# Performance work log

Measured on AMD Instinct MI355X. Metric: run time of the kernel, lower is better.

Reference implementation:

```python
import jax, jax.numpy as jnp
import numpy as np

N = 16384            # mesh vertices at full resolution (level 3)
DEG = 8              # avg nonzeros per Laplacian row
F_IN = 3
F_HID = 128
LOCAL_LAYERS = 15
LEVEL_N = [N >> (3 - l) for l in range(4)]  # [2048, 4096, 8192, 16384]


def setup_inputs():
    key = jax.random.key(0)
    ks = iter(jax.random.split(key, 48))
    d = {}
    d['inputs'] = jax.random.normal(next(ks), (1, N, F_IN), dtype=jnp.float32)
    d['mask0'] = jnp.ones((1, N, 1), jnp.float32)
    d['mask1'] = jnp.ones((1, N, 1), jnp.float32)
    for l, n in enumerate(LEVEL_N):
        e = DEG * n
        d[f'lap{l}_rows'] = jnp.sort(jax.random.randint(next(ks), (e,), 0, n, dtype=jnp.int32))
        d[f'lap{l}_cols'] = jax.random.randint(next(ks), (e,), 0, n, dtype=jnp.int32)
        d[f'lap{l}_vals'] = 0.25 * jax.random.normal(next(ks), (e,), dtype=jnp.float32)
    e = DEG * N
    d['L_rows'] = jnp.sort(jax.random.randint(next(ks), (e,), 0, N, dtype=jnp.int32))
    d['L_cols'] = jax.random.randint(next(ks), (e,), 0, N, dtype=jnp.int32)
    d['L_vals'] = 0.25 * jax.random.normal(next(ks), (e,), dtype=jnp.float32)
    s_in = 0.577   # ~1/sqrt(F_IN)
    s_h = 0.0625   # 1/sqrt(2*F_HID)
    d['g_conv1_W'] = s_in * jax.random.normal(next(ks), (F_IN, F_HID), dtype=jnp.float32)
    d['g_conv1_b'] = jnp.zeros((F_HID,), jnp.float32)
    d['g_down_W'] = s_h * jax.random.normal(next(ks), (3, 2, 2 * F_HID, F_HID), dtype=jnp.float32)
    d['g_down_b'] = jnp.zeros((3, 2, F_HID), jnp.float32)
    d['g_lap0_W'] = s_h * jax.random.normal(next(ks), (2, 2 * F_HID, F_HID), dtype=jnp.float32)
    d['g_lap0_b'] = jnp.zeros((2, F_HID), jnp.float32)
    d['g_up_W'] = s_h * jax.random.normal(next(ks), (3, 2, 2 * F_HID, F_HID), dtype=jnp.float32)
    d['g_up_b'] = jnp.zeros((3, 2, F_HID), jnp.float32)
    d['g_conv2_W'] = s_h * jax.random.normal(next(ks), (F_HID, 2), dtype=jnp.float32)
    d['g_conv2_b'] = jnp.zeros((2,), jnp.float32)
    d['l_conv1_W'] = s_in * jax.random.normal(next(ks), (F_IN, F_HID), dtype=jnp.float32)
    d['l_conv1_b'] = jnp.zeros((F_HID,), jnp.float32)
    d['l_rn_W'] = s_h * jax.random.normal(next(ks), (LOCAL_LAYERS, 2, 2 * F_HID, F_HID), dtype=jnp.float32)
    d['l_rn_b'] = jnp.zeros((LOCAL_LAYERS, 2, F_HID), jnp.float32)
    d['l_conv2_W'] = s_h * jax.random.normal(next(ks), (F_HID, 1), dtype=jnp.float32)
    d['l_conv2_b'] = jnp.zeros((1,), jnp.float32)
    return d


def _spmm(rows, cols, vals, x):
    # y = L @ x for an n x n COO Laplacian; x: [1, n, f] (batch=1, sparse mm path)
    y = jax.ops.segment_sum(vals[:, None] * x[0, cols, :], rows, num_segments=x.shape[1])
    return y[None]


def _lap_block(lap, x, Ws, bs):
    # _LapResNet2 (num_outputs == num_inputs == 128): elu -> cat([x, Lx]) -> 1x1 conv, residual
    inp = x
    for j in range(Ws.shape[0]):
        x = jax.nn.elu(x)
        x = jnp.concatenate([x, _spmm(lap[0], lap[1], lap[2], x)], axis=-1) @ Ws[j] + bs[j]
    return x + inp


def _avg_block(mask, x, Ws, bs):
    # _AvgResNet2: elu -> cat([x, masked global average]) -> 1x1 conv, residual
    inp = x
    denom = jnp.sum(mask, axis=1, keepdims=True)
    for j in range(Ws.shape[0]):
        x = jax.nn.elu(x)
        avg = jnp.sum(x * mask, axis=1, keepdims=True) / denom
        x = jnp.concatenate([x, jnp.broadcast_to(avg, x.shape)], axis=-1) @ Ws[j] + bs[j]
    return x + inp


def _maxpool2(x):
    # MaxPool1d(2, stride=2) along the node dim
    b, n, f = x.shape
    return x.reshape(b, n // 2, 2, f).max(axis=2)


def _forward(inputs, mask0, mask1, lap0_vals, lap1_vals, lap2_vals, lap3_vals, L_vals,
             g_conv1_W, g_conv1_b, g_down_W, g_down_b, g_lap0_W, g_lap0_b,
             g_up_W, g_up_b, g_conv2_W, g_conv2_b,
             l_conv1_W, l_conv1_b, l_rn_W, l_rn_b, l_conv2_W, l_conv2_b,
             lap0_rows, lap0_cols, lap1_rows, lap1_cols, lap2_rows, lap2_cols,
             lap3_rows, lap3_cols, L_rows, L_cols):
    laps = [(lap0_rows, lap0_cols, lap0_vals), (lap1_rows, lap1_cols, lap1_vals),
            (lap2_rows, lap2_cols, lap2_vals), (lap3_rows, lap3_cols, lap3_vals)]
    # ----- global net: EfficientCascade (naive max-pool cascade, 4 levels) -----
    # (mask0 is only max-pooled in torch; _LapResNet2 ignores it, so it does not affect math)
    x = inputs @ g_conv1_W + g_conv1_b
    down = []
    for k, i in enumerate((3, 2, 1)):
        down.append(x)
        x = _lap_block(laps[i], x, g_down_W[k], g_down_b[k])
        x = _maxpool2(x)
    x = _lap_block(laps[0], x, g_lap0_W, g_lap0_b)
    for i in (1, 2, 3):
        x = jnp.repeat(x, 2, axis=1)      # F.interpolate(scale_factor=2), nearest
        x = x + down[-i]                  # channels equal -> plain residual add
        x = _lap_block(laps[i], x, g_up_W[i - 1], g_up_b[i - 1])
    swg = jax.nn.elu(x) @ g_conv2_W + g_conv2_b + inputs[:, :, :2]  # + repeating_expand(inputs, 2)
    # ----- local net: LapDeepModel, 15 alternating Lap / global-avg resblocks -----
    L = (L_rows, L_cols, L_vals)
    y = inputs @ l_conv1_W + l_conv1_b
    for i in range(LOCAL_LAYERS):
        if i % 2 == 0:
            y = _lap_block(L, y, l_rn_W[i], l_rn_b[i])
        else:
            y = _avg_block(mask1, y, l_rn_W[i], l_rn_b[i])
    score_local = jax.nn.elu(y) @ l_conv2_W + l_conv2_b + inputs[:, :, :1]
    # ----- combine -----
    score_global = swg[:, :, :1]
    weight_global = jax.nn.sigmoid(swg[:, :, :-1])  # out_features=1 -> same first channel
    score_final = weight_global * score_global + (1.0 - weight_global) * score_local
    return jnp.concatenate([score_global, score_local, score_final], axis=1)


def reference(inputs, mask0, mask1, lap0_rows, lap0_cols, lap0_vals,
              lap1_rows, lap1_cols, lap1_vals, lap2_rows, lap2_cols, lap2_vals,
              lap3_rows, lap3_cols, lap3_vals, L_rows, L_cols, L_vals,
              g_conv1_W, g_conv1_b, g_down_W, g_down_b, g_lap0_W, g_lap0_b,
              g_up_W, g_up_b, g_conv2_W, g_conv2_b,
              l_conv1_W, l_conv1_b, l_rn_W, l_rn_b, l_conv2_W, l_conv2_b):
    return _forward(inputs, mask0, mask1, lap0_vals, lap1_vals, lap2_vals, lap3_vals, L_vals,
                    g_conv1_W, g_conv1_b, g_down_W, g_down_b, g_lap0_W, g_lap0_b,
                    g_up_W, g_up_b, g_conv2_W, g_conv2_b,
                    l_conv1_W, l_conv1_b, l_rn_W, l_rn_b, l_conv2_W, l_conv2_b,
                    lap0_rows, lap0_cols, lap1_rows, lap1_cols, lap2_rows, lap2_cols,
                    lap3_rows, lap3_cols, L_rows, L_cols)
```

## Files before the change

kernel.cpp:

```cpp
#include <hip/hip_runtime.h>

#define F 128
#define SPAD 136
#define NR 32

typedef __attribute__((ext_vector_type(8))) short short8;
typedef __attribute__((ext_vector_type(16))) float f32x16;
typedef unsigned long long ull;

__device__ __forceinline__ float elu_f(float x) {
    return x > 0.f ? x : __expf(x) - 1.f;
}
__device__ __forceinline__ ushort f2bf(float x) {
    unsigned u = __float_as_uint(x);
    u = (u + 0x7FFFu + ((u >> 16) & 1u)) >> 16;
    return (ushort)u;
}
__device__ __forceinline__ float bf2f(ushort u) {
    return __uint_as_float((unsigned)u << 16);
}
__device__ __forceinline__ void bfma8(float* a, float v, short8 u) {
#pragma unroll
    for (int i = 0; i < 8; ++i) a[i] += v * bf2f((ushort)u[i]);
}

struct SetupArgs {
    const float* ws0; const float* ws1; const float* ws2; const float* ws3;
    ushort* wd0; ushort* wd1; ushort* wd2; ushort* wd3;
    const int* rows0; const int* rows1; const int* rows2; const int* rows3; const int* rows4;
    int* rp0; int* rp1; int* rp2; int* rp3; int* rp4;
    const float* mask; float* den; float* acc;
};

__global__ __launch_bounds__(256) void setup_kernel(SetupArgs s) {
    __shared__ ushort tile[16384];
    int b = blockIdx.x, t = threadIdx.x;
    if (b < 88) {
        const float* src; ushort* dst; int lb;
        if (b < 12)      { src = s.ws0; dst = s.wd0; lb = b; }
        else if (b < 16) { src = s.ws1; dst = s.wd1; lb = b - 12; }
        else if (b < 28) { src = s.ws2; dst = s.wd2; lb = b - 16; }
        else             { src = s.ws3; dst = s.wd3; lb = b - 28; }
        src += (size_t)lb * 16384; dst += (size_t)lb * 16384;
        for (int idx = t; idx < 16384; idx += 256) {
            int k = idx >> 7, nn = idx & 127;
            int k0 = k >> 4, rk = k & 15, j = rk & 7, lh = rk >> 3;
            int n0 = nn >> 5, ll = nn & 31;
            tile[((k0 * 4 + n0) * 64 + lh * 32 + ll) * 8 + j] = f2bf(src[idx]);
        }
        __syncthreads();
        ull* td = (ull*)dst; const ull* ts = (const ull*)tile;
        for (int i = t; i < 4096; i += 256) td[i] = ts[i];
    } else if (b < 273) {
        int tid = (b - 88) * 256 + t;
        const int ns[5] = {2048, 4096, 8192, 16384, 16384};
        const int es[5] = {16384, 32768, 65536, 131072, 131072};
        const int* rowsA[5] = {s.rows0, s.rows1, s.rows2, s.rows3, s.rows4};
        int* rpA[5] = {s.rp0, s.rp1, s.rp2, s.rp3, s.rp4};
        int base = 0;
        for (int lv = 0; lv < 5; ++lv) {
            int cnt = ns[lv] + 1;
            if (tid < base + cnt) {
                int r = tid - base;
                const int* rows = rowsA[lv]; int e = es[lv];
                int lo = 0, hi = e;
                while (lo < hi) { int mid = (lo + hi) >> 1; if (rows[mid] < r) lo = mid + 1; else hi = mid; }
                rpA[lv][r] = lo;
                return;
            }
            base += cnt;
        }
    } else {
        __shared__ float red[256];
        float ssum = 0.f;
        for (int i = t; i < 16384; i += 256) ssum += s.mask[i];
        red[t] = ssum; __syncthreads();
        for (int st = 128; st > 0; st >>= 1) { if (t < st) red[t] += red[t + st]; __syncthreads(); }
        if (t == 0) s.den[0] = red[0];
        for (int i = t; i < 14336; i += 256) s.acc[i] = 0.f;
    }
}

__global__ void conv1_dual(const float* __restrict__ in,
                           const float* __restrict__ Wg, const float* __restrict__ bg,
                           const float* __restrict__ Wl, const float* __restrict__ bl,
                           float* __restrict__ og, ushort* __restrict__ eg,
                           float* __restrict__ ol, ushort* __restrict__ el, int n) {
    int id = blockIdx.x * 256 + threadIdx.x;
    if (id >= n * F) return;
    int r = id >> 7, c = id & 127;
    float x0 = in[r * 3 + 0], x1 = in[r * 3 + 1], x2 = in[r * 3 + 2];
    float g = x0 * Wg[c] + x1 * Wg[F + c] + x2 * Wg[2 * F + c] + bg[c];
    float lo = x0 * Wl[c] + x1 * Wl[F + c] + x2 * Wl[2 * F + c] + bl[c];
    og[id] = g;  eg[id] = f2bf(elu_f(g));
    ol[id] = lo; el[id] = f2bf(elu_f(lo));
}

struct LArgs {
    const ushort* EA; const float* RES; float* OUT; ushort* EAOUT;
    const int* rowptr; const int* cols; const float* vals;
    const ushort* Wp; const float* bias;
    const float* accin; const float* den;
    const float* mask; float* accout;
    float* EO; ushort* EE; const float* SKIP;
    int epi;
    int fin;
    const float* Finp; const ushort* FEB0;
    const float* FgW2; const float* Fgb2; const float* FlW2; const float* Flb2;
    float* Fout;
};

__device__ __forceinline__ void layer_body(const LArgs& a, int blk, ushort* SS, float* FS) {
    const int t = threadIdx.x;
    const int rbase = blk * NR;
    const int w = t >> 6, l = t & 63, m = l & 31, kh = l >> 5;
    const int col = w * 32 + m;
    const bool lap = (a.rowptr != nullptr);
    const bool avg = (a.accin != nullptr);

    short8 afrag[8];
    {
        const ushort* ear = a.EA + (size_t)(rbase + m) * F + kh * 8;
#pragma unroll
        for (int ki = 0; ki < 8; ++ki) afrag[ki] = *(const short8*)(ear + ki * 16);
    }

    if (lap) {
        const int grp = t >> 3, l8 = t & 7;
        const short8* EA8 = (const short8*)a.EA;
        const int chunk = l8 * 2;
        int row = rbase + grp;
        int e0 = a.rowptr[row], e1 = a.rowptr[row + 1];
        float acc0[16], acc1[16];
#pragma unroll
        for (int i = 0; i < 16; ++i) { acc0[i] = 0.f; acc1[i] = 0.f; }
        int e = e0;
        for (; e + 4 <= e1; e += 4) {
            int c0 = a.cols[e + 0], c1 = a.cols[e + 1], c2 = a.cols[e + 2], c3 = a.cols[e + 3];
            float v0 = a.vals[e + 0], v1 = a.vals[e + 1], v2 = a.vals[e + 2], v3 = a.vals[e + 3];
            short8 u0a = EA8[(size_t)c0 * 16 + chunk], u0b = EA8[(size_t)c0 * 16 + chunk + 1];
            short8 u1a = EA8[(size_t)c1 * 16 + chunk], u1b = EA8[(size_t)c1 * 16 + chunk + 1];
            short8 u2a = EA8[(size_t)c2 * 16 + chunk], u2b = EA8[(size_t)c2 * 16 + chunk + 1];
            short8 u3a = EA8[(size_t)c3 * 16 + chunk], u3b = EA8[(size_t)c3 * 16 + chunk + 1];
            bfma8(acc0, v0, u0a); bfma8(acc0 + 8, v0, u0b);
            bfma8(acc1, v1, u1a); bfma8(acc1 + 8, v1, u1b);
            bfma8(acc0, v2, u2a); bfma8(acc0 + 8, v2, u2b);
            bfma8(acc1, v3, u3a); bfma8(acc1 + 8, v3, u3b);
        }
        for (; e < e1; ++e) {
            int cc = a.cols[e];
            float v = a.vals[e];
            short8 ua = EA8[(size_t)cc * 16 + chunk], ub = EA8[(size_t)cc * 16 + chunk + 1];
            bfma8(acc0, v, ua); bfma8(acc0 + 8, v, ub);
        }
        short8 s0, s1;
#pragma unroll
        for (int i = 0; i < 8; ++i) {
            s0[i] = (short)f2bf(acc0[i] + acc1[i]);
            s1[i] = (short)f2bf(acc0[8 + i] + acc1[8 + i]);
        }
        *(short8*)(&SS[grp * SPAD + l8 * 16]) = s0;
        *(short8*)(&SS[grp * SPAD + l8 * 16 + 8]) = s1;
        __syncthreads();
    } else if (avg) {
        if (t < 128) {
            float s = 0.f;
#pragma unroll
            for (int r = 0; r < 8; ++r) s += a.accin[r * 128 + t];
            SS[t] = f2bf(s / a.den[0]);
        }
        __syncthreads();
    }

    f32x16 acc;
#pragma unroll
    for (int i = 0; i < 16; ++i) acc[i] = 0.f;
#pragma unroll
    for (int ki = 0; ki < 8; ++ki) {
        short8 b = *(const short8*)(a.Wp + (size_t)(((ki * 4 + w) * 64 + l) * 8));
        acc = __builtin_amdgcn_mfma_f32_32x32x16_bf16(afrag[ki], b, acc, 0, 0, 0);
    }
    if (lap || avg) {
        const ushort* esr = lap ? &SS[m * SPAD + kh * 8] : &SS[kh * 8];
#pragma unroll
        for (int ki = 0; ki < 8; ++ki) {
            short8 aa = *(const short8*)(esr + ki * 16);
            short8 b = *(const short8*)(a.Wp + 16384 + (size_t)(((ki * 4 + w) * 64 + l) * 8));
            acc = __builtin_amdgcn_mfma_f32_32x32x16_bf16(aa, b, acc, 0, 0, 0);
        }
    }

    const float bv = a.bias[col];
    float outv[16];
#pragma unroll
    for (int reg = 0; reg < 16; ++reg) {
        int r = (reg & 3) + 8 * (reg >> 2) + 4 * kh;
        size_t rg = (size_t)(rbase + r);
        float v = acc[reg] + bv;
        if (a.RES) v += a.RES[rg * F + col];
        outv[reg] = v;
        if (a.OUT) a.OUT[rg * F + col] = v;
        if (a.EAOUT) a.EAOUT[rg * F + col] = f2bf(elu_f(v));
    }
    if (a.accout) {
        float p = 0.f;
#pragma unroll
        for (int reg = 0; reg < 16; ++reg) {
            int r = (reg & 3) + 8 * (reg >> 2) + 4 * kh;
            p += elu_f(outv[reg]) * a.mask[rbase + r];
        }
        p += __shfl_xor(p, 32, 64);
        if (l < 32) atomicAdd(a.accout + (blk & 7) * 128 + col, p);
    }
    if (a.epi == 1) {
        int rb2 = rbase >> 1;
#pragma unroll
        for (int q = 0; q < 4; ++q)
#pragma unroll
            for (int e2 = 0; e2 < 2; ++e2) {
                float pv = fmaxf(outv[q * 4 + e2 * 2], outv[q * 4 + e2 * 2 + 1]);
                size_t idx = (size_t)(rb2 + q * 4 + kh * 2 + e2) * F + col;
                a.EO[idx] = pv;
                a.EE[idx] = f2bf(elu_f(pv));
            }
    } else if (a.epi == 2) {
#pragma unroll
        for (int reg = 0; reg < 16; ++reg) {
            int r = (reg & 3) + 8 * (reg >> 2) + 4 * kh;
            size_t R0 = (size_t)(2 * (rbase + r)) * F + col;
            float v0 = outv[reg] + a.SKIP[R0];
            float v1 = outv[reg] + a.SKIP[R0 + F];
            a.EO[R0] = v0;     a.EO[R0 + F] = v1;
            a.EE[R0] = f2bf(elu_f(v0)); a.EE[R0 + F] = f2bf(elu_f(v1));
        }
    }
    if (a.fin) {
        __syncthreads();
        if (t < 64) FS[t] = 0.f;
        __syncthreads();
        const float lw = a.FlW2[col];
#pragma unroll
        for (int reg = 0; reg < 16; ++reg) {
            int r = (reg & 3) + 8 * (reg >> 2) + 4 * kh;
            atomicAdd(&FS[r], elu_f(outv[reg]) * lw);
        }
        for (int idx = t; idx < 32 * 128; idx += 256) {
            int r = idx >> 7, cc = idx & 127;
            atomicAdd(&FS[32 + r], bf2f(a.FEB0[(size_t)(rbase + r) * F + cc]) * a.FgW2[2 * cc]);
        }
        __syncthreads();
        if (t < 32) {
            int rg = rbase + t;
            float base = a.Finp[rg * 3 + 0];
            float sg = FS[32 + t] + a.Fgb2[0] + base;
            float sl = FS[t] + a.Flb2[0] + base;
            float wg = 1.f / (1.f + __expf(-sg));
            a.Fout[rg] = sg;
            a.Fout[16384 + rg] = sl;
            a.Fout[32768 + rg] = wg * sg + (1.f - wg) * sl;
        }
    }
}

__global__ __launch_bounds__(256)
void dual_layer(LArgs A, LArgs B, int nA) {
    __shared__ ushort SS[NR * SPAD];
    __shared__ float FS[64];
    bool isA = (int)blockIdx.x < nA;
    const LArgs& a = isA ? A : B;
    int blk = isA ? blockIdx.x : blockIdx.x - nA;
    layer_body(a, blk, SS, FS);
}

extern "C" void kernel_launch(void* const* d_in, const int* in_sizes, int n_in,
                              void* d_out, int out_size, void* d_ws, size_t ws_size,
                              hipStream_t stream) {
    (void)in_sizes; (void)n_in; (void)out_size; (void)ws_size;
    const float* inputs = (const float*)d_in[0];
    const float* mask1  = (const float*)d_in[2];
    const int*   lrows[5] = {(const int*)d_in[3], (const int*)d_in[6], (const int*)d_in[9],
                             (const int*)d_in[12], (const int*)d_in[15]};
    const int*   lcols[5] = {(const int*)d_in[4], (const int*)d_in[7], (const int*)d_in[10],
                             (const int*)d_in[13], (const int*)d_in[16]};
    const float* lvals[5] = {(const float*)d_in[5], (const float*)d_in[8], (const float*)d_in[11],
                             (const float*)d_in[14], (const float*)d_in[17]};
    const float* gW1 = (const float*)d_in[18];
    const float* gb1 = (const float*)d_in[19];
    const float* gdW = (const float*)d_in[20];
    const float* gdb = (const float*)d_in[21];
    const float* glW = (const float*)d_in[22];
    const float* glb = (const float*)d_in[23];
    const float* guW = (const float*)d_in[24];
    const float* gub = (const float*)d_in[25];
    const float* gW2 = (const float*)d_in[26];
    const float* gb2 = (const float*)d_in[27];
    const float* lW1 = (const float*)d_in[28];
    const float* lb1 = (const float*)d_in[29];
    const float* lrW = (const float*)d_in[30];
    const float* lrb = (const float*)d_in[31];
    const float* lW2 = (const float*)d_in[32];
    const float* lb2 = (const float*)d_in[33];
    float* out = (float*)d_out;

    const int N = 16384;
    const int nlev[5] = {2048, 4096, 8192, 16384, 16384};

    char* ws = (char*)d_ws;
    size_t off = 0;
    auto alloc = [&](size_t bytes) -> char* {
        char* p = ws + off;
        off = (off + bytes + 255) & ~(size_t)255;
        return p;
    };
    float* BUF0 = (float*)alloc((size_t)N * F * 4);
    float* GU   = (float*)alloc((size_t)N * F * 4);
    float* G2   = (float*)alloc((size_t)N * F * 4);
    float* D8   = (float*)alloc((size_t)8192 * F * 4);
    float* D4   = (float*)alloc((size_t)4096 * F * 4);
    float* D2   = (float*)alloc((size_t)2048 * F * 4);
    float* LB   = (float*)alloc((size_t)N * F * 4);
    ushort* EB0 = (ushort*)alloc((size_t)N * F * 2);
    ushort* EG1 = (ushort*)alloc((size_t)N * F * 2);
    ushort* EG2 = (ushort*)alloc((size_t)N * F * 2);
    ushort* ED8 = (ushort*)alloc((size_t)8192 * F * 2);
    ushort* ED4 = (ushort*)alloc((size_t)4096 * F * 2);
    ushort* ED2 = (ushort*)alloc((size_t)2048 * F * 2);
    ushort* LE1 = (ushort*)alloc((size_t)N * F * 2);
    ushort* LE2 = (ushort*)alloc((size_t)N * F * 2);
    int* rp[5];
    for (int i = 0; i < 5; ++i) rp[i] = (int*)alloc((size_t)(nlev[i] + 1) * 4);
    float* ACC = (float*)alloc((size_t)14 * 8 * 128 * 4);
    float* DEN = (float*)alloc(4);
    ushort* Pd = (ushort*)alloc((size_t)12 * 16384 * 2);
    ushort* Pl = (ushort*)alloc((size_t)4  * 16384 * 2);
    ushort* Pu = (ushort*)alloc((size_t)12 * 16384 * 2);
    ushort* Pr = (ushort*)alloc((size_t)60 * 16384 * 2);

    SetupArgs sa;
    sa.ws0 = gdW; sa.ws1 = glW; sa.ws2 = guW; sa.ws3 = lrW;
    sa.wd0 = Pd;  sa.wd1 = Pl;  sa.wd2 = Pu;  sa.wd3 = Pr;
    sa.rows0 = lrows[0]; sa.rows1 = lrows[1]; sa.rows2 = lrows[2];
    sa.rows3 = lrows[3]; sa.rows4 = lrows[4];
    sa.rp0 = rp[0]; sa.rp1 = rp[1]; sa.rp2 = rp[2]; sa.rp3 = rp[3]; sa.rp4 = rp[4];
    sa.mask = mask1; sa.den = DEN; sa.acc = ACC;
    setup_kernel<<<274, 256, 0, stream>>>(sa);

    conv1_dual<<<8192, 256, 0, stream>>>(inputs, gW1, gb1, lW1, lb1, BUF0, EB0, LB, LE1, N);

    const size_t PSZ = 2 * 16384;

    auto mkL = [&](const ushort* ea, const float* res, float* o, ushort* eao,
                   int lv, const ushort* wp, const float* bias, float* accout,
                   int epi, float* eo, ushort* ee, const float* skip,
                   const float* accin, int fin) {
        LArgs x;
        x.EA = ea; x.RES = res; x.OUT = o; x.EAOUT = eao;
        x.rowptr = (lv >= 0) ? rp[lv] : nullptr;
        x.cols = (lv >= 0) ? lcols[lv] : nullptr;
        x.vals = (lv >= 0) ? lvals[lv] : nullptr;
        x.Wp = wp; x.bias = bias;
        x.accin = accin; x.den = DEN;
        x.mask = mask1; x.accout = accout;
        x.EO = eo; x.EE = ee; x.SKIP = skip; x.epi = epi;
        x.fin = fin;
        x.Finp = inputs; x.FEB0 = EB0;
        x.FgW2 = gW2; x.Fgb2 = gb2; x.FlW2 = lW2; x.Flb2 = lb2; x.Fout = out;
        return x;
    };

    LArgs gs[14]; int gn[14];
    gs[0]  = mkL(EB0, 0, 0, EG1, 3, Pd + 0 * PSZ, gdb + 0,   0, 0, 0, 0, 0, 0, 0);  gn[0]  = 16384;
    gs[1]  = mkL(EG1, BUF0, 0, 0, 3, Pd + 1 * PSZ, gdb + 128, 0, 1, D8, ED8, 0, 0, 0); gn[1] = 16384;
    gs[2]  = mkL(ED8, 0, 0, EG1, 2, Pd + 2 * PSZ, gdb + 256, 0, 0, 0, 0, 0, 0, 0);  gn[2]  = 8192;
    gs[3]  = mkL(EG1, D8, 0, 0, 2, Pd + 3 * PSZ, gdb + 384, 0, 1, D4, ED4, 0, 0, 0); gn[3]  = 8192;
    gs[4]  = mkL(ED4, 0, 0, EG1, 1, Pd + 4 * PSZ, gdb + 512, 0, 0, 0, 0, 0, 0, 0);  gn[4]  = 4096;
    gs[5]  = mkL(EG1, D4, 0, 0, 1, Pd + 5 * PSZ, gdb + 640, 0, 1, D2, ED2, 0, 0, 0); gn[5]  = 4096;
    gs[6]  = mkL(ED2, 0, 0, EG1, 0, Pl + 0 * PSZ, glb + 0,   0, 0, 0, 0, 0, 0, 0);  gn[6]  = 2048;
    gs[7]  = mkL(EG1, D2, 0, 0, 0, Pl + 1 * PSZ, glb + 128, 0, 2, GU, EG2, D4, 0, 0); gn[7] = 2048;
    gs[8]  = mkL(EG2, 0, 0, EG1, 1, Pu + 0 * PSZ, gub + 0,   0, 0, 0, 0, 0, 0, 0);  gn[8]  = 4096;
    gs[9]  = mkL(EG1, GU, 0, 0, 1, Pu + 1 * PSZ, gub + 128, 0, 2, G2, EG2, D8, 0, 0); gn[9] = 4096;
    gs[10] = mkL(EG2, 0, 0, EG1, 2, Pu + 2 * PSZ, gub + 256, 0, 0, 0, 0, 0, 0, 0);  gn[10] = 8192;
    gs[11] = mkL(EG1, G2, 0, 0, 2, Pu + 3 * PSZ, gub + 384, 0, 2, GU, EG2, BUF0, 0, 0); gn[11] = 8192;
    gs[12] = mkL(EG2, 0, 0, EG1, 3, Pu + 4 * PSZ, gub + 512, 0, 0, 0, 0, 0, 0, 0);  gn[12] = 16384;
    gs[13] = mkL(EG1, GU, 0, EB0, 3, Pu + 5 * PSZ, gub + 640, 0, 0, 0, 0, 0, 0, 0); gn[13] = 16384;

    int gi = 0;
    auto launchLap = [&](const LArgs& loc) {
        if (gi < 14) {
            int na = gn[gi] / NR;
            dual_layer<<<na + 512, 256, 0, stream>>>(gs[gi], loc, na);
            ++gi;
        } else {
            dual_layer<<<512, 256, 0, stream>>>(loc, loc, 512);
        }
    };

    for (int i = 0; i < 15; ++i) {
        const ushort* P1 = Pr + (size_t)(2 * i) * PSZ;
        const ushort* P2 = Pr + (size_t)(2 * i + 1) * PSZ;
        const float* b1 = lrb + (size_t)i * 256;
        const float* b2 = b1 + 128;
        if ((i & 1) == 0) {
            LArgs s1 = mkL(LE1, 0, 0, LE2, 4, P1, b1, 0, 0, 0, 0, 0, 0, 0);
            float* accout = (i <= 12) ? (ACC + (size_t)i * 1024) : nullptr;
            int fin = (i == 14);
            LArgs s2 = mkL(LE2, LB, fin ? nullptr : LB, fin ? nullptr : LE1, 4,
                           P2, b2, accout, 0, 0, 0, 0, 0, fin);
            launchLap(s1);
            launchLap(s2);
        } else {
            LArgs s1 = mkL(LE1, 0, 0, LE2, -1, P1, b1, ACC + (size_t)i * 1024,
                           0, 0, 0, 0, ACC + (size_t)(i - 1) * 1024, 0);
            LArgs s2 = mkL(LE2, LB, LB, LE1, -1, P2, b2, 0,
                           0, 0, 0, 0, ACC + (size_t)i * 1024, 0);
            launchLap(s1);
            launchLap(s2);
        }
    }
}
```

Baseline: 684.7 us.

## Bucket rows by degree for balanced SpMM blocks and use nontemporal memory ops

Adds a counting-sort pass, fused into the conv1 kernel, that builds per-level row permutations ordered by nonzero count. Laplacian layer blocks then process 32 rows of similar degree, so the threads in a block do not wait on one long row. It also switches column/value loads, residual/skip loads and the output stores to nontemporal variants to reduce cache pollution. The costs are an extra shared-memory sync per block, scattered row writes in the epilogue instead of contiguous ones, and nontemporal streaming of data the next layer may want to reuse from L2.

```diff
diff --git a/kernel.cpp b/kernel.cpp
--- a/kernel.cpp
+++ b/kernel.cpp
@@ -23,6 +23,10 @@
 #pragma unroll
     for (int i = 0; i < 8; ++i) a[i] += v * bf2f((ushort)u[i]);
 }
+__device__ __forceinline__ float ldnt(const float* p) { return __builtin_nontemporal_load(p); }
+__device__ __forceinline__ int   ldnti(const int* p)  { return __builtin_nontemporal_load(p); }
+__device__ __forceinline__ void stnt(float* p, float v)   { __builtin_nontemporal_store(v, p); }
+__device__ __forceinline__ void stnt(ushort* p, ushort v) { __builtin_nontemporal_store(v, p); }
 
 struct SetupArgs {
     const float* ws0; const float* ws1; const float* ws2; const float* ws3;
@@ -81,19 +85,47 @@
     }
 }
 
-__global__ void conv1_dual(const float* __restrict__ in,
-                           const float* __restrict__ Wg, const float* __restrict__ bg,
-                           const float* __restrict__ Wl, const float* __restrict__ bl,
-                           float* __restrict__ og, ushort* __restrict__ eg,
-                           float* __restrict__ ol, ushort* __restrict__ el, int n) {
-    int id = blockIdx.x * 256 + threadIdx.x;
-    if (id >= n * F) return;
-    int r = id >> 7, c = id & 127;
-    float x0 = in[r * 3 + 0], x1 = in[r * 3 + 1], x2 = in[r * 3 + 2];
-    float g = x0 * Wg[c] + x1 * Wg[F + c] + x2 * Wg[2 * F + c] + bg[c];
-    float lo = x0 * Wl[c] + x1 * Wl[F + c] + x2 * Wl[2 * F + c] + bl[c];
-    og[id] = g;  eg[id] = f2bf(elu_f(g));
-    ol[id] = lo; el[id] = f2bf(elu_f(lo));
+struct CArgs {
+    const float* in; const float* Wg; const float* bg; const float* Wl; const float* bl;
+    float* og; ushort* eg; float* ol; ushort* el;
+    const int* rp0; const int* rp1; const int* rp2; const int* rp3; const int* rp4;
+    int* pm0; int* pm1; int* pm2; int* pm3; int* pm4;
+};
+
+__global__ __launch_bounds__(256) void conv1_perm(CArgs c) {
+    int b = blockIdx.x, t = threadIdx.x;
+    if (b < 8192) {
+        int id = b * 256 + t;
+        int r = id >> 7, cc = id & 127;
+        float x0 = c.in[r * 3 + 0], x1 = c.in[r * 3 + 1], x2 = c.in[r * 3 + 2];
+        float g = x0 * c.Wg[cc] + x1 * c.Wg[F + cc] + x2 * c.Wg[2 * F + cc] + c.bg[cc];
+        float lo = x0 * c.Wl[cc] + x1 * c.Wl[F + cc] + x2 * c.Wl[2 * F + cc] + c.bl[cc];
+        c.og[id] = g;  c.eg[id] = f2bf(elu_f(g));
+        c.ol[id] = lo; c.el[id] = f2bf(elu_f(lo));
+    } else {
+        int lv = b - 8192;
+        const int ns[5] = {2048, 4096, 8192, 16384, 16384};
+        const int* rpA[5] = {c.rp0, c.rp1, c.rp2, c.rp3, c.rp4};
+        int* pmA[5] = {c.pm0, c.pm1, c.pm2, c.pm3, c.pm4};
+        int n = ns[lv];
+        const int* rp = rpA[lv];
+        int* pm = pmA[lv];
+        __shared__ int hist[64];
+        if (t < 64) hist[t] = 0;
+        __syncthreads();
+        for (int r = t; r < n; r += 256) {
+            int d = rp[r + 1] - rp[r]; if (d > 63) d = 63;
+            atomicAdd(&hist[d], 1);
+        }
+        __syncthreads();
+        if (t == 0) { int s = 0; for (int i = 0; i < 64; ++i) { int h = hist[i]; hist[i] = s; s += h; } }
+        __syncthreads();
+        for (int r = t; r < n; r += 256) {
+            int d = rp[r + 1] - rp[r]; if (d > 63) d = 63;
+            int pos = atomicAdd(&hist[d], 1);
+            pm[pos] = r;
+        }
+    }
 }
 
 struct LArgs {
@@ -103,6 +135,7 @@
     const float* accin; const float* den;
     const float* mask; float* accout;
     float* EO; ushort* EE; const float* SKIP;
+    const int* perm;
     int epi;
     int fin;
     const float* Finp; const ushort* FEB0;
@@ -110,7 +143,8 @@
     float* Fout;
 };
 
-__device__ __forceinline__ void layer_body(const LArgs& a, int blk, ushort* SS, float* FS) {
+__device__ __forceinline__ void layer_body(const LArgs& a, int blk, ushort* SS,
+                                           float* FS, int* PR) {
     const int t = threadIdx.x;
     const int rbase = blk * NR;
     const int w = t >> 6, l = t & 63, m = l & 31, kh = l >> 5;
@@ -118,9 +152,12 @@
     const bool lap = (a.rowptr != nullptr);
     const bool avg = (a.accin != nullptr);
 
+    if (t < 32) PR[t] = a.perm ? a.perm[rbase + t] : rbase + t;
+    __syncthreads();
+
     short8 afrag[8];
     {
-        const ushort* ear = a.EA + (size_t)(rbase + m) * F + kh * 8;
+        const ushort* ear = a.EA + (size_t)PR[m] * F + kh * 8;
 #pragma unroll
         for (int ki = 0; ki < 8; ++ki) afrag[ki] = *(const short8*)(ear + ki * 16);
     }
@@ -129,15 +166,17 @@
         const int grp = t >> 3, l8 = t & 7;
         const short8* EA8 = (const short8*)a.EA;
         const int chunk = l8 * 2;
-        int row = rbase + grp;
+        int row = PR[grp];
         int e0 = a.rowptr[row], e1 = a.rowptr[row + 1];
         float acc0[16], acc1[16];
 #pragma unroll
         for (int i = 0; i < 16; ++i) { acc0[i] = 0.f; acc1[i] = 0.f; }
         int e = e0;
         for (; e + 4 <= e1; e += 4) {
-            int c0 = a.cols[e + 0], c1 = a.cols[e + 1], c2 = a.cols[e + 2], c3 = a.cols[e + 3];
-            float v0 = a.vals[e + 0], v1 = a.vals[e + 1], v2 = a.vals[e + 2], v3 = a.vals[e + 3];
+            int c0 = ldnti(a.cols + e + 0), c1 = ldnti(a.cols + e + 1);
+            int c2 = ldnti(a.cols + e + 2), c3 = ldnti(a.cols + e + 3);
+            float v0 = ldnt(a.vals + e + 0), v1 = ldnt(a.vals + e + 1);
+            float v2 = ldnt(a.vals + e + 2), v3 = ldnt(a.vals + e + 3);
             short8 u0a = EA8[(size_t)c0 * 16 + chunk], u0b = EA8[(size_t)c0 * 16 + chunk + 1];
             short8 u1a = EA8[(size_t)c1 * 16 + chunk], u1b = EA8[(size_t)c1 * 16 + chunk + 1];
             short8 u2a = EA8[(size_t)c2 * 16 + chunk], u2b = EA8[(size_t)c2 * 16 + chunk + 1];
@@ -148,8 +187,8 @@
             bfma8(acc1, v3, u3a); bfma8(acc1 + 8, v3, u3b);
         }
         for (; e < e1; ++e) {
-            int cc = a.cols[e];
-            float v = a.vals[e];
+            int cc = ldnti(a.cols + e);
+            float v = ldnt(a.vals + e);
             short8 ua = EA8[(size_t)cc * 16 + chunk], ub = EA8[(size_t)cc * 16 + chunk + 1];
             bfma8(acc0, v, ua); bfma8(acc0 + 8, v, ub);
         }
@@ -195,19 +234,19 @@
 #pragma unroll
     for (int reg = 0; reg < 16; ++reg) {
         int r = (reg & 3) + 8 * (reg >> 2) + 4 * kh;
-        size_t rg = (size_t)(rbase + r);
+        size_t rg = (size_t)PR[r];
         float v = acc[reg] + bv;
-        if (a.RES) v += a.RES[rg * F + col];
+        if (a.RES) v += ldnt(a.RES + rg * F + col);
         outv[reg] = v;
-        if (a.OUT) a.OUT[rg * F + col] = v;
-        if (a.EAOUT) a.EAOUT[rg * F + col] = f2bf(elu_f(v));
+        if (a.OUT) stnt(a.OUT + rg * F + col, v);
+        if (a.EAOUT) stnt(a.EAOUT + rg * F + col, f2bf(elu_f(v)));
     }
     if (a.accout) {
         float p = 0.f;
 #pragma unroll
         for (int reg = 0; reg < 16; ++reg) {
             int r = (reg & 3) + 8 * (reg >> 2) + 4 * kh;
-            p += elu_f(outv[reg]) * a.mask[rbase + r];
+            p += elu_f(outv[reg]) * a.mask[PR[r]];
         }
         p += __shfl_xor(p, 32, 64);
         if (l < 32) atomicAdd(a.accout + (blk & 7) * 128 + col, p);
@@ -220,18 +259,18 @@
             for (int e2 = 0; e2 < 2; ++e2) {
                 float pv = fmaxf(outv[q * 4 + e2 * 2], outv[q * 4 + e2 * 2 + 1]);
                 size_t idx = (size_t)(rb2 + q * 4 + kh * 2 + e2) * F + col;
-                a.EO[idx] = pv;
-                a.EE[idx] = f2bf(elu_f(pv));
+                stnt(a.EO + idx, pv);
+                stnt(a.EE + idx, f2bf(elu_f(pv)));
             }
     } else if (a.epi == 2) {
 #pragma unroll
         for (int reg = 0; reg < 16; ++reg) {
             int r = (reg & 3) + 8 * (reg >> 2) + 4 * kh;
             size_t R0 = (size_t)(2 * (rbase + r)) * F + col;
-            float v0 = outv[reg] + a.SKIP[R0];
-            float v1 = outv[reg] + a.SKIP[R0 + F];
-            a.EO[R0] = v0;     a.EO[R0 + F] = v1;
-            a.EE[R0] = f2bf(elu_f(v0)); a.EE[R0 + F] = f2bf(elu_f(v1));
+            float v0 = outv[reg] + ldnt(a.SKIP + R0);
+            float v1 = outv[reg] + ldnt(a.SKIP + R0 + F);
+            stnt(a.EO + R0, v0);     stnt(a.EO + R0 + F, v1);
+            stnt(a.EE + R0, f2bf(elu_f(v0))); stnt(a.EE + R0 + F, f2bf(elu_f(v1)));
         }
     }
     if (a.fin) {
@@ -246,11 +285,11 @@
         }
         for (int idx = t; idx < 32 * 128; idx += 256) {
             int r = idx >> 7, cc = idx & 127;
-            atomicAdd(&FS[32 + r], bf2f(a.FEB0[(size_t)(rbase + r) * F + cc]) * a.FgW2[2 * cc]);
+            atomicAdd(&FS[32 + r], bf2f(a.FEB0[(size_t)PR[r] * F + cc]) * a.FgW2[2 * cc]);
         }
         __syncthreads();
         if (t < 32) {
-            int rg = rbase + t;
+            int rg = PR[t];
             float base = a.Finp[rg * 3 + 0];
             float sg = FS[32 + t] + a.Fgb2[0] + base;
             float sl = FS[t] + a.Flb2[0] + base;
@@ -266,10 +305,11 @@
 void dual_layer(LArgs A, LArgs B, int nA) {
     __shared__ ushort SS[NR * SPAD];
     __shared__ float FS[64];
+    __shared__ int PR[32];
     bool isA = (int)blockIdx.x < nA;
     const LArgs& a = isA ? A : B;
     int blk = isA ? blockIdx.x : blockIdx.x - nA;
-    layer_body(a, blk, SS, FS);
+    layer_body(a, blk, SS, FS, PR);
 }
 
 extern "C" void kernel_launch(void* const* d_in, const int* in_sizes, int n_in,
@@ -329,6 +369,8 @@
     ushort* LE2 = (ushort*)alloc((size_t)N * F * 2);
     int* rp[5];
     for (int i = 0; i < 5; ++i) rp[i] = (int*)alloc((size_t)(nlev[i] + 1) * 4);
+    int* pm[5];
+    for (int i = 0; i < 5; ++i) pm[i] = (int*)alloc((size_t)nlev[i] * 4);
     float* ACC = (float*)alloc((size_t)14 * 8 * 128 * 4);
     float* DEN = (float*)alloc(4);
     ushort* Pd = (ushort*)alloc((size_t)12 * 16384 * 2);
@@ -345,14 +387,19 @@
     sa.mask = mask1; sa.den = DEN; sa.acc = ACC;
     setup_kernel<<<274, 256, 0, stream>>>(sa);
 
-    conv1_dual<<<8192, 256, 0, stream>>>(inputs, gW1, gb1, lW1, lb1, BUF0, EB0, LB, LE1, N);
+    CArgs ca;
+    ca.in = inputs; ca.Wg = gW1; ca.bg = gb1; ca.Wl = lW1; ca.bl = lb1;
+    ca.og = BUF0; ca.eg = EB0; ca.ol = LB; ca.el = LE1;
+    ca.rp0 = rp[0]; ca.rp1 = rp[1]; ca.rp2 = rp[2]; ca.rp3 = rp[3]; ca.rp4 = rp[4];
+    ca.pm0 = pm[0]; ca.pm1 = pm[1]; ca.pm2 = pm[2]; ca.pm3 = pm[3]; ca.pm4 = pm[4];
+    conv1_perm<<<8197, 256, 0, stream>>>(ca);
 
     const size_t PSZ = 2 * 16384;
 
     auto mkL = [&](const ushort* ea, const float* res, float* o, ushort* eao,
                    int lv, const ushort* wp, const float* bias, float* accout,
                    int epi, float* eo, ushort* ee, const float* skip,
-                   const float* accin, int fin) {
+                   const float* accin, int fin, const int* perm) {
         LArgs x;
         x.EA = ea; x.RES = res; x.OUT = o; x.EAOUT = eao;
         x.rowptr = (lv >= 0) ? rp[lv] : nullptr;
@@ -361,7 +408,7 @@
         x.Wp = wp; x.bias = bias;
         x.accin = accin; x.den = DEN;
         x.mask = mask1; x.accout = accout;
-        x.EO = eo; x.EE = ee; x.SKIP = skip; x.epi = epi;
+        x.EO = eo; x.EE = ee; x.SKIP = skip; x.perm = perm; x.epi = epi;
         x.fin = fin;
         x.Finp = inputs; x.FEB0 = EB0;
         x.FgW2 = gW2; x.Fgb2 = gb2; x.FlW2 = lW2; x.Flb2 = lb2; x.Fout = out;
@@ -369,20 +416,20 @@
     };
 
     LArgs gs[14]; int gn[14];
-    gs[0]  = mkL(EB0, 0, 0, EG1, 3, Pd + 0 * PSZ, gdb + 0,   0, 0, 0, 0, 0, 0, 0);  gn[0]  = 16384;
-    gs[1]  = mkL(EG1, BUF0, 0, 0, 3, Pd + 1 * PSZ, gdb + 128, 0, 1, D8, ED8, 0, 0, 0); gn[1] = 16384;
-    gs[2]  = mkL(ED8, 0, 0, EG1, 2, Pd + 2 * PSZ, gdb + 256, 0, 0, 0, 0, 0, 0, 0);  gn[2]  = 8192;
-    gs[3]  = mkL(EG1, D8, 0, 0, 2, Pd + 3 * PSZ, gdb + 384, 0, 1, D4, ED4, 0, 0, 0); gn[3]  = 8192;
-    gs[4]  = mkL(ED4, 0, 0, EG1, 1, Pd + 4 * PSZ, gdb + 512, 0, 0, 0, 0, 0, 0, 0);  gn[4]  = 4096;
-    gs[5]  = mkL(EG1, D4, 0, 0, 1, Pd + 5 * PSZ, gdb + 640, 0, 1, D2, ED2, 0, 0, 0); gn[5]  = 4096;
-    gs[6]  = mkL(ED2, 0, 0, EG1, 0, Pl + 0 * PSZ, glb + 0,   0, 0, 0, 0, 0, 0, 0);  gn[6]  = 2048;
-    gs[7]  = mkL(EG1, D2, 0, 0, 0, Pl + 1 * PSZ, glb + 128, 0, 2, GU, EG2, D4, 0, 0); gn[7] = 2048;
-    gs[8]  = mkL(EG2, 0, 0, EG1, 1, Pu + 0 * PSZ, gub + 0,   0, 0, 0, 0, 0, 0, 0);  gn[8]  = 4096;
-    gs[9]  = mkL(EG1, GU, 0, 0, 1, Pu + 1 * PSZ, gub + 128, 0, 2, G2, EG2, D8, 0, 0); gn[9] = 4096;
-    gs[10] = mkL(EG2, 0, 0, EG1, 2, Pu + 2 * PSZ, gub + 256, 0, 0, 0, 0, 0, 0, 0);  gn[10] = 8192;
-    gs[11] = mkL(EG1, G2, 0, 0, 2, Pu + 3 * PSZ, gub + 384, 0, 2, GU, EG2, BUF0, 0, 0); gn[11] = 8192;
-    gs[12] = mkL(EG2, 0, 0, EG1, 3, Pu + 4 * PSZ, gub + 512, 0, 0, 0, 0, 0, 0, 0);  gn[12] = 16384;
-    gs[13] = mkL(EG1, GU, 0, EB0, 3, Pu + 5 * PSZ, gub + 640, 0, 0, 0, 0, 0, 0, 0); gn[13] = 16384;
+    gs[0]  = mkL(EB0, 0, 0, EG1, 3, Pd + 0 * PSZ, gdb + 0,   0, 0, 0, 0, 0, 0, 0, pm[3]);  gn[0]  = 16384;
+    gs[1]  = mkL(EG1, BUF0, 0, 0, 3, Pd + 1 * PSZ, gdb + 128, 0, 1, D8, ED8, 0, 0, 0, 0); gn[1] = 16384;
+    gs[2]  = mkL(ED8, 0, 0, EG1, 2, Pd + 2 * PSZ, gdb + 256, 0, 0, 0, 0, 0, 0, 0, pm[2]);  gn[2]  = 8192;
+    gs[3]  = mkL(EG1, D8, 0, 0, 2, Pd + 3 * PSZ, gdb + 384, 0, 1, D4, ED4, 0, 0, 0, 0); gn[3]  = 8192;
+    gs[4]  = mkL(ED4, 0, 0, EG1, 1, Pd + 4 * PSZ, gdb + 512, 0, 0, 0, 0, 0, 0, 0, pm[1]);  gn[4]  = 4096;
+    gs[5]  = mkL(EG1, D4, 0, 0, 1, Pd + 5 * PSZ, gdb + 640, 0, 1, D2, ED2, 0, 0, 0, 0); gn[5]  = 4096;
+    gs[6]  = mkL(ED2, 0, 0, EG1, 0, Pl + 0 * PSZ, glb + 0,   0, 0, 0, 0, 0, 0, 0, pm[0]);  gn[6]  = 2048;
+    gs[7]  = mkL(EG1, D2, 0, 0, 0, Pl + 1 * PSZ, glb + 128, 0, 2, GU, EG2, D4, 0, 0, 0); gn[7] = 2048;
+    gs[8]  = mkL(EG2, 0, 0, EG1, 1, Pu + 0 * PSZ, gub + 0,   0, 0, 0, 0, 0, 0, 0, pm[1]);  gn[8]  = 4096;
+    gs[9]  = mkL(EG1, GU, 0, 0, 1, Pu + 1 * PSZ, gub + 128, 0, 2, G2, EG2, D8, 0, 0, 0); gn[9] = 4096;
+    gs[10] = mkL(EG2, 0, 0, EG1, 2, Pu + 2 * PSZ, gub + 256, 0, 0, 0, 0, 0, 0, 0, pm[2]);  gn[10] = 8192;
+    gs[11] = mkL(EG1, G2, 0, 0, 2, Pu + 3 * PSZ, gub + 384, 0, 2, GU, EG2, BUF0, 0, 0, 0); gn[11] = 8192;
+    gs[12] = mkL(EG2, 0, 0, EG1, 3, Pu + 4 * PSZ, gub + 512, 0, 0, 0, 0, 0, 0, 0, pm[3]);  gn[12] = 16384;
+    gs[13] = mkL(EG1, GU, 0, EB0, 3, Pu + 5 * PSZ, gub + 640, 0, 0, 0, 0, 0, 0, 0, pm[3]); gn[13] = 16384;
 
     int gi = 0;
     auto launchLap = [&](const LArgs& loc) {
@@ -401,18 +448,18 @@
         const float* b1 = lrb + (size_t)i * 256;
         const float* b2 = b1 + 128;
         if ((i & 1) == 0) {
-            LArgs s1 = mkL(LE1, 0, 0, LE2, 4, P1, b1, 0, 0, 0, 0, 0, 0, 0);
+            LArgs s1 = mkL(LE1, 0, 0, LE2, 4, P1, b1, 0, 0, 0, 0, 0, 0, 0, pm[4]);
             float* accout = (i <= 12) ? (ACC + (size_t)i * 1024) : nullptr;
             int fin = (i == 14);
             LArgs s2 = mkL(LE2, LB, fin ? nullptr : LB, fin ? nullptr : LE1, 4,
-                           P2, b2, accout, 0, 0, 0, 0, 0, fin);
+                           P2, b2, accout, 0, 0, 0, 0, 0, fin, pm[4]);
             launchLap(s1);
             launchLap(s2);
         } else {
             LArgs s1 = mkL(LE1, 0, 0, LE2, -1, P1, b1, ACC + (size_t)i * 1024,
-                           0, 0, 0, 0, ACC + (size_t)(i - 1) * 1024, 0);
+                           0, 0, 0, 0, ACC + (size_t)(i - 1) * 1024, 0, 0);
             LArgs s2 = mkL(LE2, LB, LB, LE1, -1, P2, b2, 0,
-                           0, 0, 0, 0, ACC + (size_t)i * 1024, 0);
+                           0, 0, 0, 0, ACC + (size_t)i * 1024, 0, 0);
             launchLap(s1);
             launchLap(s2);
         }
```

Measured after the change: 861.6 us. 25.8% more time.
